# Kernel optimization log

Hardware: AMD Instinct MI355X
Metric: run time of the kernel (lower is better)

Reference implementation:

```python
import jax, jax.numpy as jnp
import numpy as np

DN = ('NCHW', 'OIHW', 'NCHW')

def conv(x, w, b, stride, pad):
    y = jax.lax.conv_general_dilated(x, w, (stride, stride), ((pad, pad), (pad, pad)), dimension_numbers=DN)
    return y + b[None, :, None, None]

def conv_transpose(x, w, b, stride, pad):
    # w has torch ConvTranspose2d layout (Cin, Cout, kh, kw)
    k = w.shape[2]
    w_f = jnp.transpose(w[:, :, ::-1, ::-1], (1, 0, 2, 3))  # -> OIHW, spatially flipped
    p = k - 1 - pad
    y = jax.lax.conv_general_dilated(x, w_f, (1, 1), ((p, p), (p, p)), lhs_dilation=(stride, stride), dimension_numbers=DN)
    return y + b[None, :, None, None]

def setup_inputs() -> dict:
    key = jax.random.key(0)
    ks = jax.random.split(key, 16)
    K, D = 512, 64
    s = 0.05
    inp = {
        'x': jax.random.uniform(ks[0], (32, 3, 256, 256), dtype=jnp.float32),
        'enc_w1': jax.random.normal(ks[1], (32, 3, 4, 4), jnp.float32) * s,
        'enc_b1': jnp.zeros((32,), jnp.float32),
        'enc_w2': jax.random.normal(ks[2], (64, 32, 4, 4), jnp.float32) * s,
        'enc_b2': jnp.zeros((64,), jnp.float32),
        'enc_w3': jax.random.normal(ks[3], (D, 64, 3, 3), jnp.float32) * s,
        'enc_b3': jnp.zeros((D,), jnp.float32),
        'codebook': jax.random.uniform(ks[4], (K, D), jnp.float32, -1.0 / K, 1.0 / K),
        'dec_w1': jax.random.normal(ks[5], (D, 64, 4, 4), jnp.float32) * s,   # ConvT (Cin,Cout,k,k)
        'dec_b1': jnp.zeros((64,), jnp.float32),
        'dec_w2': jax.random.normal(ks[6], (64, 32, 4, 4), jnp.float32) * s,  # ConvT
        'dec_b2': jnp.zeros((32,), jnp.float32),
        'dec_w3': jax.random.normal(ks[7], (3, 32, 3, 3), jnp.float32) * s,
        'dec_b3': jnp.zeros((3,), jnp.float32),
    }
    return inp

COMMITMENT_COST = 0.25

def reference(x, enc_w1, enc_b1, enc_w2, enc_b2, enc_w3, enc_b3, codebook,
              dec_w1, dec_b1, dec_w2, dec_b2, dec_w3, dec_b3):
    sg = jax.lax.stop_gradient
    # encoder
    h = jax.nn.relu(conv(x, enc_w1, enc_b1, 2, 1))
    h = jax.nn.relu(conv(h, enc_w2, enc_b2, 2, 1))
    z = conv(h, enc_w3, enc_b3, 1, 1)  # [B, D, H/4, W/4]
    # vector quantizer
    D = codebook.shape[1]
    z_perm = jnp.transpose(z, (0, 2, 3, 1))  # BHWD
    flat = z_perm.reshape(-1, D)  # [N, D]
    dist = jnp.sum(flat * flat, axis=1, keepdims=True) - 2.0 * (flat @ codebook.T) + jnp.sum(codebook * codebook, axis=1)  # [N, K]
    idx = jnp.argmin(dist, axis=1)
    q = codebook[idx].reshape(z_perm.shape)
    q = jnp.transpose(q, (0, 3, 1, 2))  # BDHW
    vq_loss = jnp.mean((sg(q) - z) ** 2) + COMMITMENT_COST * jnp.mean((q - sg(z)) ** 2)
    q_st = z + sg(q - z)  # straight-through
    # decoder
    h = jax.nn.relu(conv_transpose(q_st, dec_w1, dec_b1, 2, 1))
    h = jax.nn.relu(conv_transpose(h, dec_w2, dec_b2, 2, 1))
    recon = jax.nn.sigmoid(conv(h, dec_w3, dec_b3, 1, 1))
    return recon, vq_loss
```

## Files before the change

### kernel.cpp

```cpp
#include <hip/hip_runtime.h>

typedef unsigned short u16;
typedef unsigned int u32;
typedef __attribute__((ext_vector_type(8))) short bf16x8;
typedef __attribute__((ext_vector_type(4))) float f32x4;

#define MFMA(a, b, c) __builtin_amdgcn_mfma_f32_16x16x32_bf16(a, b, c, 0, 0, 0)

__device__ __forceinline__ float b2f(u32 lo16) {
  union { u32 i; float f; } v; v.i = lo16 << 16; return v.f;
}
__device__ __forceinline__ u16 f2b(float f) {
  union { float f; u32 i; } v; v.f = f;
  return (u16)((v.i + 0x7fffu + ((v.i >> 16) & 1u)) >> 16);
}
__device__ __forceinline__ u16 f2bt(float f) {
  union { float f; u32 i; } v; v.f = f;
  return (u16)(v.i >> 16);
}
__device__ __forceinline__ bf16x8 ld8(const u16* p) { return *(const bf16x8*)p; }

__global__ void prep_k(const float* __restrict__ ew1, const float* __restrict__ ew2,
                       const float* __restrict__ ew3, const float* __restrict__ dw1,
                       const float* __restrict__ dw2, const float* __restrict__ dw3,
                       const float* __restrict__ cb,
                       float* W1, u16* Bp2, u16* Bp3, u16* BpT1, u16* BpT2,
                       u16* Bpd3, u16* Bpvq, float* cnorm, float* loss) {
  int tid = blockIdx.x * blockDim.x + threadIdx.x;
  int nth = gridDim.x * blockDim.x;
  for (int i = tid; i < 1536; i += nth) {
    int oc = i & 31; int r = i >> 5; int kw = r & 3; r >>= 2; int kh = r & 3; int ic = r >> 2;
    W1[i] = ew1[((oc*3 + ic)*4 + kh)*4 + kw];
  }
  for (int i = tid; i < 32768; i += nth) {
    int j = i & 7, li = (i >> 3) & 63, nt = (i >> 9) & 3, t = i >> 11;
    int ic = 8*(li >> 4) + j, oc = 16*nt + (li & 15), kh = t >> 2, kw = t & 3;
    Bp2[i] = f2b(ew2[((oc*32 + ic)*4 + kh)*4 + kw]);
  }
  for (int i = tid; i < 36864; i += nth) {
    int j = i & 7, li = (i >> 3) & 63, nt = (i >> 9) & 3, kc = (i >> 11) & 1, t = i >> 12;
    int ic = 32*kc + 8*(li >> 4) + j, oc = 16*nt + (li & 15), kh = t / 3, kw = t % 3;
    Bp3[i] = f2b(ew3[((oc*64 + ic)*3 + kh)*3 + kw]);
  }
  for (int i = tid; i < 65536; i += nth) {
    int j = i & 7, li = (i >> 3) & 63, nt = (i >> 9) & 3, kc = (i >> 11) & 1,
        t = (i >> 12) & 3, p = i >> 14;
    int a = p >> 1, b = p & 1;
    int ky = (1 - a) + 2*(t >> 1), kx = (1 - b) + 2*(t & 1);
    int ic = 32*kc + 8*(li >> 4) + j, oc = 16*nt + (li & 15);
    BpT1[i] = f2b(dw1[((ic*64 + oc)*4 + ky)*4 + kx]);
  }
  for (int i = tid; i < 32768; i += nth) {
    int j = i & 7, li = (i >> 3) & 63, nt = (i >> 9) & 1, kc = (i >> 10) & 1,
        t = (i >> 11) & 3, p = i >> 13;
    int a = p >> 1, b = p & 1;
    int ky = (1 - a) + 2*(t >> 1), kx = (1 - b) + 2*(t & 1);
    int ic = 32*kc + 8*(li >> 4) + j, oc = 16*nt + (li & 15);
    BpT2[i] = f2b(dw2[((ic*32 + oc)*4 + ky)*4 + kx]);
  }
  for (int i = tid; i < 4608; i += nth) {
    int j = i & 7, li = (i >> 3) & 63, t = i >> 9;
    int n = li & 15, ic = 8*(li >> 4) + j, kh = t / 3, kw = t % 3;
    Bpd3[i] = (n < 3) ? f2b(dw3[((n*32 + ic)*3 + kh)*3 + kw]) : (u16)0;
  }
  for (int i = tid; i < 32768; i += nth) {
    int j = i & 7, li = (i >> 3) & 63, nt = (i >> 9) & 31, kc = i >> 14;
    int d = 32*kc + 8*(li >> 4) + j, code = 16*nt + (li & 15);
    Bpvq[i] = f2b(cb[code*64 + d]);
  }
  for (int k = tid; k < 512; k += nth) {
    float s = 0.f;
    for (int d = 0; d < 64; ++d) { float c = cb[k*64 + d]; s += c*c; }
    cnorm[k] = s;
  }
  if (tid == 0) *loss = 0.f;
}

__global__ __launch_bounds__(256) void conv1_k(
    const float* __restrict__ x, const float* __restrict__ W1,
    const float* __restrict__ b1, u16* __restrict__ h1) {
  __shared__ float ins[3*18*36];
  int Tx = blockIdx.x, Ty = blockIdx.y, b = blockIdx.z;
  int tid = threadIdx.x;
  for (int i = tid; i < 3*18*36; i += 256) {
    int c = i % 36; int r = (i / 36) % 18; int ic = i / 648;
    int iy = 16*Ty - 1 + r, ix = 32*Tx - 2 + c;
    float v = 0.f;
    if ((unsigned)iy < 256u && (unsigned)ix < 256u)
      v = x[((size_t)(b*3 + ic)*256 + iy)*256 + ix];
    ins[i] = v;
  }
  __syncthreads();
  int posg = tid & 31, ocg = tid >> 5;
  int Y = posg >> 2, Xg = posg & 3;
  int oc0 = ocg * 4;
  float acc[4][4];
#pragma unroll
  for (int j = 0; j < 4; ++j) { float bv = b1[oc0 + j];
#pragma unroll
    for (int e = 0; e < 4; ++e) acc[j][e] = bv; }
  for (int ic = 0; ic < 3; ++ic)
#pragma unroll
    for (int kh = 0; kh < 4; ++kh) {
      const float* row = &ins[ic*648 + (2*Y + kh)*36 + 8*Xg];
      float win[12];
#pragma unroll
      for (int t = 0; t < 12; ++t) win[t] = row[t];
#pragma unroll
      for (int kw = 0; kw < 4; ++kw) {
        const float* wp = &W1[((ic*4 + kh)*4 + kw)*32 + oc0];
        float w0 = wp[0], w1 = wp[1], w2 = wp[2], w3 = wp[3];
#pragma unroll
        for (int e = 0; e < 4; ++e) {
          float v = win[2*e + kw + 1];
          acc[0][e] += w0*v; acc[1][e] += w1*v; acc[2][e] += w2*v; acc[3][e] += w3*v;
        }
      }
    }
  int oy = 8*Ty + Y;
  int oxb = 16*Tx + 4*Xg;
#pragma unroll
  for (int e = 0; e < 4; ++e) {
    u16* op = &h1[((size_t)(b*128 + oy)*128 + oxb + e)*32 + oc0];
#pragma unroll
    for (int j = 0; j < 4; ++j) op[j] = f2b(fmaxf(acc[j][e], 0.f));
  }
}

__global__ __launch_bounds__(256) void conv2_k(
    const u16* __restrict__ h1, const u16* __restrict__ Bp2,
    const float* __restrict__ eb2, u16* __restrict__ h2) {
  __shared__ u16 lds[2448*8];
  int Tx = blockIdx.x, Ty = blockIdx.y, img = blockIdx.z;
  int tid = threadIdx.x;
  for (int i = tid; i < 2448; i += 256) {
    int c = i & 3; int x = (i >> 2) % 34; int row = (i >> 2) / 34;
    int iy = 16*Ty - 1 + row, ix = 32*Tx - 1 + x;
    f32x4 v = {0,0,0,0};
    if ((unsigned)iy < 128u && (unsigned)ix < 128u)
      v = *(const f32x4*)(h1 + (((size_t)(img*128 + iy)*128 + ix)*32 + c*8));
    *(f32x4*)(lds + ((row*4 + c)*34 + x)*8) = v;
  }
  __syncthreads();
  int w = tid >> 6, l = tid & 63, lg = l >> 4, lc = l & 15;
  f32x4 acc[2][4];
#pragma unroll
  for (int nt = 0; nt < 4; ++nt) {
    float bv = eb2[nt*16 + lc];
    acc[0][nt] = (f32x4){bv,bv,bv,bv}; acc[1][nt] = (f32x4){bv,bv,bv,bv};
  }
#pragma unroll
  for (int t = 0; t < 16; ++t) {
    int kh = t >> 2, kw = t & 3;
    bf16x8 a0 = ld8(lds + (((2*w + kh)*4 + lg)*34 + 2*lc + kw)*8);
    bf16x8 a1 = ld8(lds + (((2*(w+4) + kh)*4 + lg)*34 + 2*lc + kw)*8);
    const u16* bp = Bp2 + t*2048 + l*8;
    bf16x8 b0 = ld8(bp), b1 = ld8(bp + 512), b2v = ld8(bp + 1024), b3v = ld8(bp + 1536);
    acc[0][0] = MFMA(a0, b0, acc[0][0]); acc[0][1] = MFMA(a0, b1, acc[0][1]);
    acc[0][2] = MFMA(a0, b2v, acc[0][2]); acc[0][3] = MFMA(a0, b3v, acc[0][3]);
    acc[1][0] = MFMA(a1, b0, acc[1][0]); acc[1][1] = MFMA(a1, b1, acc[1][1]);
    acc[1][2] = MFMA(a1, b2v, acc[1][2]); acc[1][3] = MFMA(a1, b3v, acc[1][3]);
  }
#pragma unroll
  for (int m = 0; m < 2; ++m) {
    int oy = 8*Ty + w + m*4;
#pragma unroll
    for (int nt = 0; nt < 4; ++nt)
#pragma unroll
      for (int r = 0; r < 4; ++r) {
        int e = 4*lg + r;
        h2[((size_t)(img*64 + oy)*64 + 16*Tx + e)*64 + nt*16 + lc] =
            f2b(fmaxf(acc[m][nt][r], 0.f));
      }
  }
}

__global__ __launch_bounds__(256) void conv3e_k(
    const u16* __restrict__ h2, const u16* __restrict__ Bp3,
    const float* __restrict__ eb3, u16* __restrict__ z) {
  __shared__ u16 lds[1440*8];
  int Tx = blockIdx.x, Ty = blockIdx.y, img = blockIdx.z;
  int tid = threadIdx.x;
  for (int i = tid; i < 1440; i += 256) {
    int c = i & 7; int x = (i >> 3) % 18; int row = (i >> 3) / 18;
    int iy = 8*Ty - 1 + row, ix = 16*Tx - 1 + x;
    f32x4 v = {0,0,0,0};
    if ((unsigned)iy < 64u && (unsigned)ix < 64u)
      v = *(const f32x4*)(h2 + (((size_t)(img*64 + iy)*64 + ix)*64 + c*8));
    *(f32x4*)(lds + ((row*8 + c)*18 + x)*8) = v;
  }
  __syncthreads();
  int w = tid >> 6, l = tid & 63, lg = l >> 4, lc = l & 15;
  f32x4 acc[2][4];
#pragma unroll
  for (int nt = 0; nt < 4; ++nt) {
    float bv = eb3[nt*16 + lc];
    acc[0][nt] = (f32x4){bv,bv,bv,bv}; acc[1][nt] = (f32x4){bv,bv,bv,bv};
  }
#pragma unroll
  for (int t = 0; t < 9; ++t) {
    int kh = t / 3, kw = t % 3;
#pragma unroll
    for (int kc = 0; kc < 2; ++kc) {
      bf16x8 a0 = ld8(lds + (((w + kh)*8 + kc*4 + lg)*18 + lc + kw)*8);
      bf16x8 a1 = ld8(lds + (((w + 4 + kh)*8 + kc*4 + lg)*18 + lc + kw)*8);
      const u16* bp = Bp3 + (t*2 + kc)*2048 + l*8;
      bf16x8 b0 = ld8(bp), b1 = ld8(bp + 512), b2v = ld8(bp + 1024), b3v = ld8(bp + 1536);
      acc[0][0] = MFMA(a0, b0, acc[0][0]); acc[0][1] = MFMA(a0, b1, acc[0][1]);
      acc[0][2] = MFMA(a0, b2v, acc[0][2]); acc[0][3] = MFMA(a0, b3v, acc[0][3]);
      acc[1][0] = MFMA(a1, b0, acc[1][0]); acc[1][1] = MFMA(a1, b1, acc[1][1]);
      acc[1][2] = MFMA(a1, b2v, acc[1][2]); acc[1][3] = MFMA(a1, b3v, acc[1][3]);
    }
  }
#pragma unroll
  for (int m = 0; m < 2; ++m) {
    int oy = 8*Ty + w + m*4;
#pragma unroll
    for (int nt = 0; nt < 4; ++nt)
#pragma unroll
      for (int r = 0; r < 4; ++r) {
        int e = 4*lg + r;
        z[((size_t)(img*64 + oy)*64 + 16*Tx + e)*64 + nt*16 + lc] = f2b(acc[m][nt][r]);
      }
  }
}

__global__ __launch_bounds__(256) void vqm_k(
    const u16* __restrict__ z, const u16* __restrict__ Bpvq,
    const float* __restrict__ cnorm, const float* __restrict__ cbf,
    u16* __restrict__ q, float* __restrict__ loss) {
  __shared__ u16 cbl[32768];
  __shared__ float cnl[512];
  __shared__ int idxl[64];
  __shared__ float red[256];
  int tid = threadIdx.x;
  for (int i = tid; i < 4096; i += 256)
    *(f32x4*)(cbl + i*8) = *(const f32x4*)(Bpvq + i*8);
  for (int i = tid; i < 512; i += 256) cnl[i] = cnorm[i];
  __syncthreads();
  int w = tid >> 6, l = tid & 63, lg = l >> 4, lc = l & 15;
  int wglobal = blockIdx.x*4 + w;
  float lsum = 0.f;
  for (int it = 0; it < 8; ++it) {
    int mf = wglobal + it*1024;
    size_t P = (size_t)mf * 16;
    bf16x8 a0 = ld8(z + (P + lc)*64 + lg*8);
    bf16x8 a1 = ld8(z + (P + lc)*64 + 32 + lg*8);
    float best[4] = {1e30f, 1e30f, 1e30f, 1e30f};
    int bidx[4] = {0, 0, 0, 0};
    for (int nt = 0; nt < 32; ++nt) {
      f32x4 acc = {0,0,0,0};
      acc = MFMA(a0, ld8(cbl + (nt*64 + l)*8), acc);
      acc = MFMA(a1, ld8(cbl + ((32 + nt)*64 + l)*8), acc);
      float cn = cnl[nt*16 + lc];
      int code = nt*16 + lc;
#pragma unroll
      for (int r = 0; r < 4; ++r) {
        float dist = cn - 2.f*acc[r];
        if (dist < best[r]) { best[r] = dist; bidx[r] = code; }
      }
    }
#pragma unroll
    for (int r = 0; r < 4; ++r) {
      float b = best[r]; int bi = bidx[r];
      for (int m = 1; m < 16; m <<= 1) {
        float ob = __shfl_xor(b, m);
        int oi = __shfl_xor(bi, m);
        if (ob < b || (ob == b && oi < bi)) { b = ob; bi = oi; }
      }
      if (lc == 0) idxl[w*16 + lg*4 + r] = bi;
    }
    int m = lc, ch0 = lg*16;
    int id = idxl[w*16 + m];
    const float* crow = cbf + (size_t)id*64 + ch0;
    const u16* zp = z + (P + m)*64 + ch0;
    u32* qp = (u32*)(q + (P + m)*64 + ch0);
#pragma unroll
    for (int c = 0; c < 16; c += 2) {
      float c0 = crow[c], c1 = crow[c+1];
      float d0 = c0 - b2f(zp[c]), d1 = c1 - b2f(zp[c+1]);
      lsum += d0*d0 + d1*d1;
      qp[c >> 1] = (u32)f2bt(c0) | ((u32)f2bt(c1) << 16);
    }
  }
  red[tid] = lsum;
  __syncthreads();
  for (int s = 128; s > 0; s >>= 1) {
    if (tid < s) red[tid] += red[tid + s];
    __syncthreads();
  }
  if (tid == 0) atomicAdd(loss, red[0] * (1.25f / 8388608.f));
}

__global__ __launch_bounds__(256) void convt1_k(
    const u16* __restrict__ q, const u16* __restrict__ BpT1,
    const float* __restrict__ db1, u16* __restrict__ d1) {
  __shared__ u16 lds[864*8];
  int Tx = blockIdx.x, Ty = blockIdx.y, img = blockIdx.z;
  int X0 = 16*Tx, P0 = 4*Ty;
  int tid = threadIdx.x;
  for (int i = tid; i < 864; i += 256) {
    int c = i & 7; int x = (i >> 3) % 18; int row = (i >> 3) / 18;
    int iy = P0 - 1 + row, ix = X0 - 1 + x;
    f32x4 v = {0,0,0,0};
    if ((unsigned)iy < 64u && (unsigned)ix < 64u)
      v = *(const f32x4*)(q + (((size_t)(img*64 + iy)*64 + ix)*64 + c*8));
    *(f32x4*)(lds + ((row*8 + c)*18 + x)*8) = v;
  }
  __syncthreads();
  int w = tid >> 6, l = tid & 63, lg = l >> 4, lc = l & 15;
  int a = w & 1, bp_ = w >> 1;
  f32x4 acc[4][4];
#pragma unroll
  for (int nt = 0; nt < 4; ++nt) {
    float bv = db1[nt*16 + lc];
#pragma unroll
    for (int m = 0; m < 4; ++m) acc[m][nt] = (f32x4){bv,bv,bv,bv};
  }
  const u16* bbase = BpT1 + (size_t)(a*2 + bp_)*16384;
#pragma unroll
  for (int t = 0; t < 4; ++t) {
    int kyi = t >> 1, kxi = t & 1;
#pragma unroll
    for (int kc = 0; kc < 2; ++kc) {
      const u16* bp = bbase + (t*2 + kc)*2048 + l*8;
      bf16x8 b0 = ld8(bp), b1 = ld8(bp + 512), b2v = ld8(bp + 1024), b3v = ld8(bp + 1536);
      int xg = lc + bp_ - kxi + 1;
#pragma unroll
      for (int m = 0; m < 4; ++m) {
        int rowg = m + a - kyi + 1;
        bf16x8 av = ld8(lds + ((rowg*8 + kc*4 + lg)*18 + xg)*8);
        acc[m][0] = MFMA(av, b0, acc[m][0]);
        acc[m][1] = MFMA(av, b1, acc[m][1]);
        acc[m][2] = MFMA(av, b2v, acc[m][2]);
        acc[m][3] = MFMA(av, b3v, acc[m][3]);
      }
    }
  }
#pragma unroll
  for (int m = 0; m < 4; ++m) {
    int oy = 2*(P0 + m) + a;
#pragma unroll
    for (int nt = 0; nt < 4; ++nt)
#pragma unroll
      for (int r = 0; r < 4; ++r) {
        int e = 4*lg + r;
        int ox = 2*(X0 + e) + bp_;
        d1[((size_t)(img*128 + oy)*128 + ox)*64 + nt*16 + lc] =
            f2bt(fmaxf(acc[m][nt][r], 0.f));
      }
  }
}

__global__ __launch_bounds__(256) void tail_k(
    const u16* __restrict__ d1, const u16* __restrict__ BpT2,
    const float* __restrict__ db2, const u16* __restrict__ Bpd3,
    const float* __restrict__ db3, float* __restrict__ out) {
  __shared__ u16 lds[1224*8];
  __shared__ u16 d2s[2048*8];
  int Tx = blockIdx.x, Ty = blockIdx.y, img = blockIdx.z;
  int DX0 = 30*Tx - 1, DY0 = 14*Ty - 1;
  int IY0 = (DY0 - 2) >> 1, IX0 = (DX0 - 2) >> 1;
  int tid = threadIdx.x;
  for (int i = tid; i < 1224; i += 256) {
    int x = i % 17; int rc = i / 17; int c = rc & 7; int row = rc >> 3;
    int iy = IY0 + 1 + row, ix = IX0 + 1 + x;
    f32x4 v = {0,0,0,0};
    if ((unsigned)iy < 128u && (unsigned)ix < 128u)
      v = *(const f32x4*)(d1 + (((size_t)(img*128 + iy)*128 + ix)*64 + c*8));
    *(f32x4*)(lds + ((row*8 + c)*17 + x)*8) = v;
  }
  __syncthreads();
  int w = tid >> 6, l = tid & 63, lg = l >> 4, lc = l & 15;
  {
    int a = w & 1, bp_ = w >> 1;
    int py0 = (DY0 + ((DY0 ^ a) & 1)) >> 1;
    int px0 = (DX0 + ((DX0 ^ bp_) & 1)) >> 1;
    f32x4 acc[8][2];
#pragma unroll
    for (int nt = 0; nt < 2; ++nt) {
      float bv = db2[nt*16 + lc];
#pragma unroll
      for (int m = 0; m < 8; ++m) acc[m][nt] = (f32x4){bv,bv,bv,bv};
    }
    const u16* bbase = BpT2 + (size_t)(a*2 + bp_)*8192;
#pragma unroll
    for (int t = 0; t < 4; ++t) {
      int kyi = t >> 1, kxi = t & 1;
#pragma unroll
      for (int kc = 0; kc < 2; ++kc) {
        const u16* bb = bbase + (t*2 + kc)*1024 + l*8;
        bf16x8 b0 = ld8(bb), b1 = ld8(bb + 512);
        int xg = px0 + lc + bp_ - kxi - IX0 - 1;
#pragma unroll
        for (int m = 0; m < 8; ++m) {
          int rowg = py0 + m + a - kyi - IY0 - 1;
          bf16x8 av = ld8(lds + ((rowg*8 + kc*4 + lg)*17 + xg)*8);
          acc[m][0] = MFMA(av, b0, acc[m][0]);
          acc[m][1] = MFMA(av, b1, acc[m][1]);
        }
      }
    }
#pragma unroll
    for (int m = 0; m < 8; ++m) {
      int py = py0 + m; int oy = 2*py + a;
      int ly = oy - DY0;
#pragma unroll
      for (int nt = 0; nt < 2; ++nt)
#pragma unroll
        for (int r = 0; r < 4; ++r) {
          int e = 4*lg + r;
          int ox = 2*(px0 + e) + bp_;
          int lx = ox - DX0;
          float v = fmaxf(acc[m][nt][r], 0.f);
          if ((unsigned)oy >= 256u || (unsigned)ox >= 256u) v = 0.f;
          int oc = nt*16 + lc;
          int oi = (((ly*4 + (oc >> 3))*32 + lx)) ^ ((lx >> 3) & 3);
          d2s[oi*8 + (oc & 7)] = f2bt(v);
        }
    }
  }
  __syncthreads();
  bf16x8 bw[9];
#pragma unroll
  for (int t = 0; t < 9; ++t) bw[t] = ld8(Bpd3 + t*512 + l*8);
  float bv3 = (lc < 3) ? db3[lc] : 0.f;
  for (int yy = w; yy < 14; yy += 4) {
    int gy = DY0 + 1 + yy;
#pragma unroll
    for (int xf = 0; xf < 2; ++xf) {
      f32x4 acc = {bv3, bv3, bv3, bv3};
#pragma unroll
      for (int t = 0; t < 9; ++t) {
        int kh = t / 3, kw = t % 3;
        int lx = xf*16 + lc + kw; if (lx > 31) lx = 31;
        int oi = (((yy + kh)*4 + lg)*32 + lx) ^ ((lx >> 3) & 3);
        bf16x8 av = ld8(d2s + oi*8);
        acc = MFMA(av, bw[t], acc);
      }
      if (lc < 3 && (unsigned)gy < 256u) {
#pragma unroll
        for (int r = 0; r < 4; ++r) {
          int e = 4*lg + r;
          int xi = xf*16 + e;
          int gx = DX0 + 1 + xi;
          if (xi < 30 && (unsigned)gx < 256u)
            out[((size_t)(img*3 + lc)*256 + gy)*256 + gx] = 1.f / (1.f + expf(-acc[r]));
        }
      }
    }
  }
}

extern "C" void kernel_launch(void* const* d_in, const int* in_sizes, int n_in,
                              void* d_out, int out_size, void* d_ws, size_t ws_size,
                              hipStream_t stream) {
  const float* x   = (const float*)d_in[0];
  const float* ew1 = (const float*)d_in[1];
  const float* eb1 = (const float*)d_in[2];
  const float* ew2 = (const float*)d_in[3];
  const float* eb2 = (const float*)d_in[4];
  const float* ew3 = (const float*)d_in[5];
  const float* eb3 = (const float*)d_in[6];
  const float* cb  = (const float*)d_in[7];
  const float* dw1 = (const float*)d_in[8];
  const float* db1 = (const float*)d_in[9];
  const float* dw2 = (const float*)d_in[10];
  const float* db2 = (const float*)d_in[11];
  const float* dw3 = (const float*)d_in[12];
  const float* db3 = (const float*)d_in[13];
  float* out = (float*)d_out;

  char* ws = (char*)d_ws;
  const size_t MB = 1048576;
  u16* h1 = (u16*)ws;
  u16* q  = (u16*)ws;
  u16* d1 = (u16*)(ws + 16*MB);
  u16* h2 = (u16*)(ws + 32*MB);
  u16* z  = (u16*)(ws + 48*MB);
  char* wp = ws + 80*MB;
  float* W1   = (float*)wp;  wp += 6144;
  u16*  Bp2   = (u16*)wp;    wp += 65536;
  u16*  Bp3   = (u16*)wp;    wp += 73728;
  u16*  BpT1  = (u16*)wp;    wp += 131072;
  u16*  BpT2  = (u16*)wp;    wp += 65536;
  u16*  Bpd3  = (u16*)wp;    wp += 9216;
  u16*  Bpvq  = (u16*)wp;    wp += 65536;
  float* cnorm = (float*)wp; wp += 2048;
  float* loss = out + 6291456;

  prep_k<<<64, 256, 0, stream>>>(ew1, ew2, ew3, dw1, dw2, dw3, cb,
                                 W1, Bp2, Bp3, BpT1, BpT2, Bpd3, Bpvq, cnorm, loss);
  conv1_k<<<dim3(8, 16, 32), 256, 0, stream>>>(x, W1, eb1, h1);
  conv2_k<<<dim3(4, 8, 32), 256, 0, stream>>>(h1, Bp2, eb2, h2);
  conv3e_k<<<dim3(4, 8, 32), 256, 0, stream>>>(h2, Bp3, eb3, z);
  vqm_k<<<256, 256, 0, stream>>>(z, Bpvq, cnorm, cb, q, loss);
  convt1_k<<<dim3(4, 16, 32), 256, 0, stream>>>(q, BpT1, db1, d1);
  tail_k<<<dim3(9, 19, 32), 256, 0, stream>>>(d1, BpT2, db2, Bpd3, db3, out);
}
```

Before: 318.6 us.

## Shrink tail tile height and restructure ConvT2/conv3 LDS layout by parity quadrant

```diff
diff --git a/kernel.cpp b/kernel.cpp
--- a/kernel.cpp
+++ b/kernel.cpp
@@ -356,68 +356,73 @@
     const u16* __restrict__ d1, const u16* __restrict__ BpT2,
     const float* __restrict__ db2, const u16* __restrict__ Bpd3,
     const float* __restrict__ db3, float* __restrict__ out) {
-  __shared__ u16 lds[1224*8];
-  __shared__ u16 d2s[2048*8];
+  __shared__ u16 d1s[680*8];
+  __shared__ u16 d2q[8192];
   int Tx = blockIdx.x, Ty = blockIdx.y, img = blockIdx.z;
-  int DX0 = 30*Tx - 1, DY0 = 14*Ty - 1;
-  int IY0 = (DY0 - 2) >> 1, IX0 = (DX0 - 2) >> 1;
+  int DX0 = 30*Tx - 1, DY0 = 6*Ty - 1;
+  int IYB = 3*Ty, IXB = 15*Tx;
   int tid = threadIdx.x;
-  for (int i = tid; i < 1224; i += 256) {
+  for (int i = tid; i < 680; i += 256) {
     int x = i % 17; int rc = i / 17; int c = rc & 7; int row = rc >> 3;
-    int iy = IY0 + 1 + row, ix = IX0 + 1 + x;
+    int iy = IYB - 1 + row, ix = IXB - 1 + x;
     f32x4 v = {0,0,0,0};
     if ((unsigned)iy < 128u && (unsigned)ix < 128u)
       v = *(const f32x4*)(d1 + (((size_t)(img*128 + iy)*128 + ix)*64 + c*8));
-    *(f32x4*)(lds + ((row*8 + c)*17 + x)*8) = v;
+    *(f32x4*)(d1s + ((row*8 + c)*17 + x)*8) = v;
   }
   __syncthreads();
   int w = tid >> 6, l = tid & 63, lg = l >> 4, lc = l & 15;
   {
-    int a = w & 1, bp_ = w >> 1;
-    int py0 = (DY0 + ((DY0 ^ a) & 1)) >> 1;
-    int px0 = (DX0 + ((DX0 ^ bp_) & 1)) >> 1;
-    f32x4 acc[8][2];
+    int a = w & 1, b = w >> 1;
+    f32x4 acc[4][2];
 #pragma unroll
     for (int nt = 0; nt < 2; ++nt) {
       float bv = db2[nt*16 + lc];
 #pragma unroll
-      for (int m = 0; m < 8; ++m) acc[m][nt] = (f32x4){bv,bv,bv,bv};
-    }
-    const u16* bbase = BpT2 + (size_t)(a*2 + bp_)*8192;
-#pragma unroll
-    for (int t = 0; t < 4; ++t) {
-      int kyi = t >> 1, kxi = t & 1;
+      for (int m = 0; m < 4; ++m) acc[m][nt] = (f32x4){bv,bv,bv,bv};
+    }
+    const u16* bbase = BpT2 + (size_t)(a*2 + b)*8192;
+#pragma unroll
+    for (int kxi = 0; kxi < 2; ++kxi) {
+      int xg = lc - kxi + 1;
 #pragma unroll
       for (int kc = 0; kc < 2; ++kc) {
-        const u16* bb = bbase + (t*2 + kc)*1024 + l*8;
-        bf16x8 b0 = ld8(bb), b1 = ld8(bb + 512);
-        int xg = px0 + lc + bp_ - kxi - IX0 - 1;
-#pragma unroll
-        for (int m = 0; m < 8; ++m) {
-          int rowg = py0 + m + a - kyi - IY0 - 1;
-          bf16x8 av = ld8(lds + ((rowg*8 + kc*4 + lg)*17 + xg)*8);
-          acc[m][0] = MFMA(av, b0, acc[m][0]);
-          acc[m][1] = MFMA(av, b1, acc[m][1]);
+        bf16x8 av[5];
+#pragma unroll
+        for (int rr = 0; rr < 5; ++rr)
+          av[rr] = ld8(d1s + ((rr*8 + kc*4 + lg)*17 + xg)*8);
+#pragma unroll
+        for (int kyi = 0; kyi < 2; ++kyi) {
+          int t = kyi*2 + kxi;
+          const u16* bb = bbase + (t*2 + kc)*1024 + l*8;
+          bf16x8 b0 = ld8(bb), b1 = ld8(bb + 512);
+#pragma unroll
+          for (int m = 0; m < 4; ++m) {
+            acc[m][0] = MFMA(av[m + 1 - kyi], b0, acc[m][0]);
+            acc[m][1] = MFMA(av[m + 1 - kyi], b1, acc[m][1]);
+          }
         }
       }
     }
-#pragma unroll
-    for (int m = 0; m < 8; ++m) {
-      int py = py0 + m; int oy = 2*py + a;
-      int ly = oy - DY0;
-#pragma unroll
-      for (int nt = 0; nt < 2; ++nt)
+    int oyb = DY0 + (1 - a);
+    int oxb = DX0 + (1 - b) + 8*lg;
+    bool cm[4];
+#pragma unroll
+    for (int r = 0; r < 4; ++r) cm[r] = (unsigned)(oxb + 2*r) < 256u;
+    int base = (a*2 + b)*2048 + lg*128 + lc;
+    int ntk = (lg & 1);
+#pragma unroll
+    for (int m = 0; m < 4; ++m) {
+      bool rm = (unsigned)(oyb + 2*m) < 256u;
+#pragma unroll
+      for (int nt = 0; nt < 2; ++nt) {
+        int wb = base + m*512 + ((nt ^ ntk) << 4);
 #pragma unroll
         for (int r = 0; r < 4; ++r) {
-          int e = 4*lg + r;
-          int ox = 2*(px0 + e) + bp_;
-          int lx = ox - DX0;
-          float v = fmaxf(acc[m][nt][r], 0.f);
-          if ((unsigned)oy >= 256u || (unsigned)ox >= 256u) v = 0.f;
-          int oc = nt*16 + lc;
-          int oi = (((ly*4 + (oc >> 3))*32 + lx)) ^ ((lx >> 3) & 3);
-          d2s[oi*8 + (oc & 7)] = f2bt(v);
+          float v = (rm && cm[r]) ? fmaxf(acc[m][nt][r], 0.f) : 0.f;
+          d2q[wb + r*32] = f2bt(v);
         }
+      }
     }
   }
   __syncthreads();
@@ -425,28 +430,29 @@
 #pragma unroll
   for (int t = 0; t < 9; ++t) bw[t] = ld8(Bpd3 + t*512 + l*8);
   float bv3 = (lc < 3) ? db3[lc] : 0.f;
-  for (int yy = w; yy < 14; yy += 4) {
+#pragma unroll
+  for (int i = 0; i < 3; ++i) {
+    int u = w + 4*i;
+    int yy = u >> 1, xf = u & 1;
     int gy = DY0 + 1 + yy;
-#pragma unroll
-    for (int xf = 0; xf < 2; ++xf) {
-      f32x4 acc = {bv3, bv3, bv3, bv3};
-#pragma unroll
-      for (int t = 0; t < 9; ++t) {
-        int kh = t / 3, kw = t % 3;
-        int lx = xf*16 + lc + kw; if (lx > 31) lx = 31;
-        int oi = (((yy + kh)*4 + lg)*32 + lx) ^ ((lx >> 3) & 3);
-        bf16x8 av = ld8(d2s + oi*8);
-        acc = MFMA(av, bw[t], acc);
-      }
-      if (lc < 3 && (unsigned)gy < 256u) {
-#pragma unroll
-        for (int r = 0; r < 4; ++r) {
-          int e = 4*lg + r;
-          int xi = xf*16 + e;
-          int gx = DX0 + 1 + xi;
-          if (xi < 30 && (unsigned)gx < 256u)
-            out[((size_t)(img*3 + lc)*256 + gy)*256 + gx] = 1.f / (1.f + expf(-acc[r]));
-        }
+    f32x4 acc = {bv3, bv3, bv3, bv3};
+#pragma unroll
+    for (int t = 0; t < 9; ++t) {
+      int kh = t / 3, kw = t % 3;
+      int ly = yy + kh;
+      int lx = xf*16 + lc + kw;
+      if (lx > 31) lx = 31;
+      int quad = (1 - (ly & 1))*2 + (1 - (lx & 1));
+      int ridx = quad*2048 + (ly >> 1)*512 + (lx >> 1)*32 + ((lg*8) ^ ((lx & 8)*2));
+      acc = MFMA(ld8(d2q + ridx), bw[t], acc);
+    }
+    if (lc < 3 && (unsigned)gy < 256u) {
+#pragma unroll
+      for (int r = 0; r < 4; ++r) {
+        int xi = xf*16 + 4*lg + r;
+        int gx = DX0 + 1 + xi;
+        if (xi < 30 && (unsigned)gx < 256u)
+          out[((size_t)(img*3 + lc)*256 + gy)*256 + gx] = 1.f / (1.f + expf(-acc[r]));
       }
     }
   }
@@ -496,5 +502,5 @@
   conv3e_k<<<dim3(4, 8, 32), 256, 0, stream>>>(h2, Bp3, eb3, z);
   vqm_k<<<256, 256, 0, stream>>>(z, Bpvq, cnorm, cb, q, loss);
   convt1_k<<<dim3(4, 16, 32), 256, 0, stream>>>(q, BpT1, db1, d1);
-  tail_k<<<dim3(9, 19, 32), 256, 0, stream>>>(d1, BpT2, db2, Bpd3, db3, out);
-}
+  tail_k<<<dim3(9, 43, 32), 256, 0, stream>>>(d1, BpT2, db2, Bpd3, db3, out);
+}
```

Result: faster. 290.5 us (-8.8%).
